# Performance work log

Measured on AMD Instinct MI355X. Metric: run time of the kernel, lower is better.

The kernel has to match this reference:

```python
import jax, jax.numpy as jnp
import numpy as np

BS, SL, ENC_DIM, EDGE_DIM = 8, 256, 1024, 256
MINUS_INF = -1.0e8


def setup_inputs() -> dict:
    key = jax.random.key(0)
    ks = jax.random.split(key, 5)
    encoded_text = jax.random.normal(ks[0], (BS, SL, ENC_DIM), dtype=jnp.float32)
    mask = jnp.ones((BS, SL), dtype=jnp.int64)
    # Linear params (torch stores weight as (out, in)); scale like default init
    Wh = jax.random.normal(ks[1], (EDGE_DIM, ENC_DIM), dtype=jnp.float32) / np.sqrt(ENC_DIM)
    bh = jax.random.normal(ks[2], (EDGE_DIM,), dtype=jnp.float32) / np.sqrt(ENC_DIM)
    Wc = jax.random.normal(ks[3], (EDGE_DIM, ENC_DIM), dtype=jnp.float32) / np.sqrt(ENC_DIM)
    w_out = jax.random.normal(ks[4], (EDGE_DIM,), dtype=jnp.float32) / np.sqrt(EDGE_DIM)
    return {"encoded_text": encoded_text, "mask": mask, "Wh": Wh, "bh": bh, "Wc": Wc, "w_out": w_out}


def reference(encoded_text, mask, Wh, bh, Wc, w_out):
    # head/child projections: (bs, sl, edge_dim)
    head = jnp.einsum('bse,de->bsd', encoded_text, Wh) + bh
    child = jnp.einsum('bse,de->bsd', encoded_text, Wc)
    # Pairwise: torch code gives combined[b,i,j] = tanh(head[b,j] + child[b,i])
    combined = jnp.tanh(head[:, None, :, :] + child[:, :, None, :])  # (bs, sl, sl, edge_dim)
    edge_scores = jnp.einsum('bijd,d->bij', combined, w_out)  # (bs, sl, sl)
    float_mask = mask.astype(jnp.float32)
    minus_mask = (1.0 - float_mask) * MINUS_INF  # (bs, sl)
    edge_scores = edge_scores + minus_mask[:, :, None] + minus_mask[:, None, :]
    return edge_scores
```

## Files before the change

kernel.cpp:

```cpp
#include <hip/hip_runtime.h>
#include <hip/hip_bf16.h>
#include <stdint.h>


typedef __bf16 bf16_t;
typedef __attribute__((ext_vector_type(8))) __bf16 bf16x8;
typedef __attribute__((ext_vector_type(4))) float f32x4;

#define SL 256
#define ENC 1024
#define NTOT 512
#define N_ENC 2097152
#define N_W 262144
#define KSCALE 2.8853900817779268f

__device__ __forceinline__ void async16(void* lds, const void* g) {
  __builtin_amdgcn_global_load_lds(
      (const __attribute__((address_space(1))) uint32_t*)g,
      (__attribute__((address_space(3))) uint32_t*)lds, 16, 0, 0);
}
__device__ __forceinline__ unsigned short f32_to_bf16_rne(float f) {
  uint32_t u = __float_as_uint(f);
  return (unsigned short)((u + 0x7FFFu + ((u >> 16) & 1u)) >> 16);
}

__global__ __launch_bounds__(256)
void convert_kernel(const float* __restrict__ enc, const float* __restrict__ Wh,
                    const float* __restrict__ Wc,
                    unsigned short* __restrict__ encB, unsigned short* __restrict__ WB) {
  int gi = (blockIdx.x * 256 + threadIdx.x) * 4;
  const float* src;
  unsigned short* dst;
  int off;
  if (gi < N_ENC) {
    src = enc; off = gi; dst = encB + gi;
  } else if (gi < N_ENC + N_W) {
    src = Wh; off = gi - N_ENC; dst = WB + off;
  } else {
    src = Wc; off = gi - N_ENC - N_W; dst = WB + N_W + off;
  }
  f32x4 v = *(const f32x4*)(src + off);
  ushort4 o;
  o.x = f32_to_bf16_rne(v[0]); o.y = f32_to_bf16_rne(v[1]);
  o.z = f32_to_bf16_rne(v[2]); o.w = f32_to_bf16_rne(v[3]);
  *(ushort4*)dst = o;
}

__global__ __launch_bounds__(256)
void proj_kernel(const unsigned short* __restrict__ A, const unsigned short* __restrict__ WB,
                 const float* __restrict__ bh, float* __restrict__ hc) {
  __shared__ bf16_t As[2][64 * 32];
  __shared__ bf16_t Bs[2][64 * 32];
  const int t = threadIdx.x;
  const int wv = t >> 6, lane = t & 63;
  const int m0 = blockIdx.x * 64;
  const int n0 = blockIdx.y * 64;
  const int srow = t >> 2, schunk = t & 3;
  const int mq = (wv & 1) * 32, nq = (wv >> 1) * 32;
  const int fr = lane & 15, kq = lane >> 4;

  f32x4 acc00 = {0.f, 0.f, 0.f, 0.f};
  f32x4 acc01 = acc00, acc10 = acc00, acc11 = acc00;

  const unsigned short* gA = A + (size_t)(m0 + srow) * ENC + schunk * 8;
  const unsigned short* gB = WB + (size_t)(n0 + srow) * ENC + schunk * 8;

  async16(&As[0][wv * 512], gA);
  async16(&Bs[0][wv * 512], gB);

#pragma unroll 4
  for (int i = 0; i < 32; ++i) {
    const int buf = i & 1;
    __syncthreads();
    if (i + 1 < 32) {
      const int k1 = (i + 1) * 32;
      async16(&As[buf ^ 1][wv * 512], gA + k1);
      async16(&Bs[buf ^ 1][wv * 512], gB + k1);
    }
    bf16x8 a0 = *(const bf16x8*)&As[buf][(mq + fr) * 32 + kq * 8];
    bf16x8 a1 = *(const bf16x8*)&As[buf][(mq + 16 + fr) * 32 + kq * 8];
    bf16x8 b0 = *(const bf16x8*)&Bs[buf][(nq + fr) * 32 + kq * 8];
    bf16x8 b1 = *(const bf16x8*)&Bs[buf][(nq + 16 + fr) * 32 + kq * 8];
    acc00 = __builtin_amdgcn_mfma_f32_16x16x32_bf16(a0, b0, acc00, 0, 0, 0);
    acc01 = __builtin_amdgcn_mfma_f32_16x16x32_bf16(a0, b1, acc01, 0, 0, 0);
    acc10 = __builtin_amdgcn_mfma_f32_16x16x32_bf16(a1, b0, acc10, 0, 0, 0);
    acc11 = __builtin_amdgcn_mfma_f32_16x16x32_bf16(a1, b1, acc11, 0, 0, 0);
  }
  const int colA = n0 + nq + fr;
  const int colB = colA + 16;
  const float biasA = (colA < 256) ? bh[colA] : 0.0f;
  const float biasB = (colB < 256) ? bh[colB] : 0.0f;
#pragma unroll
  for (int r = 0; r < 4; ++r) {
    int row0 = m0 + mq + kq * 4 + r;
    int row1 = row0 + 16;
    hc[(size_t)row0 * NTOT + colA] = __builtin_amdgcn_exp2f(KSCALE * (acc00[r] + biasA));
    hc[(size_t)row0 * NTOT + colB] = __builtin_amdgcn_exp2f(KSCALE * (acc01[r] + biasB));
    hc[(size_t)row1 * NTOT + colA] = __builtin_amdgcn_exp2f(KSCALE * (acc10[r] + biasA));
    hc[(size_t)row1 * NTOT + colB] = __builtin_amdgcn_exp2f(KSCALE * (acc11[r] + biasB));
  }
}

#define LSTR 260
__global__ __launch_bounds__(256)
void edge_kernel(const float* __restrict__ hc, const float* __restrict__ wout,
                 const int* __restrict__ mask, float* __restrict__ out) {
  __shared__ float ldH[32 * LSTR];
  __shared__ float ldC[32 * LSTR];
  __shared__ float wS[256];
  __shared__ float red[256];
  const int t = threadIdx.x;
  const int b = blockIdx.z;
  const int i0 = blockIdx.y * 32;
  const int j0 = blockIdx.x * 32;
  const int sbase = b * SL;

  float w = wout[t];
  wS[t] = -2.0f * w;
  red[t] = w;

  for (int u = t; u < 32 * 64; u += 256) {
    int row = u >> 6;
    int c4 = (u & 63) << 2;
    f32x4 hv = *(const f32x4*)&hc[(size_t)(sbase + j0 + row) * NTOT + c4];
    f32x4 cv = *(const f32x4*)&hc[(size_t)(sbase + i0 + row) * NTOT + 256 + c4];
    *(f32x4*)&ldH[row * LSTR + c4] = hv;
    *(f32x4*)&ldC[row * LSTR + c4] = cv;
  }
  __syncthreads();
  for (int s = 128; s > 0; s >>= 1) {
    if (t < s) red[t] += red[t + s];
    __syncthreads();
  }
  const float S = red[0];

  const int tx = t & 15, ty = t >> 4;
  const float* hp0 = &ldH[tx * LSTR];
  const float* hp1 = &ldH[(tx + 16) * LSTR];
  const float* cp0 = &ldC[ty * LSTR];
  const float* cp1 = &ldC[(ty + 16) * LSTR];
  float a00 = 0.f, a01 = 0.f, a10 = 0.f, a11 = 0.f;

#pragma unroll 8
  for (int d = 0; d < 256; d += 4) {
    f32x4 h0 = *(const f32x4*)&hp0[d];
    f32x4 h1 = *(const f32x4*)&hp1[d];
    f32x4 c0 = *(const f32x4*)&cp0[d];
    f32x4 c1 = *(const f32x4*)&cp1[d];
    f32x4 w4 = *(const f32x4*)&wS[d];
#pragma unroll
    for (int e = 0; e < 4; ++e) {
      float he0 = h0[e], he1 = h1[e], ce0 = c0[e], ce1 = c1[e], we = w4[e];
      float r00 = __builtin_amdgcn_rcpf(ce0 * he0 + 1.0f);
      float r01 = __builtin_amdgcn_rcpf(ce0 * he1 + 1.0f);
      float r10 = __builtin_amdgcn_rcpf(ce1 * he0 + 1.0f);
      float r11 = __builtin_amdgcn_rcpf(ce1 * he1 + 1.0f);
      a00 = fmaf(we, r00, a00);
      a01 = fmaf(we, r01, a01);
      a10 = fmaf(we, r10, a10);
      a11 = fmaf(we, r11, a11);
    }
  }

  const int gi0 = sbase + i0 + ty, gi1 = gi0 + 16;
  const int gj0 = j0 + tx, gj1 = gj0 + 16;
  const float mi0 = (1.0f - (float)mask[gi0]) * -1.0e8f;
  const float mi1 = (1.0f - (float)mask[gi1]) * -1.0e8f;
  const float mj0 = (1.0f - (float)mask[sbase + gj0]) * -1.0e8f;
  const float mj1 = (1.0f - (float)mask[sbase + gj1]) * -1.0e8f;
  out[(size_t)gi0 * SL + gj0] = S + a00 + mi0 + mj0;
  out[(size_t)gi0 * SL + gj1] = S + a01 + mi0 + mj1;
  out[(size_t)gi1 * SL + gj0] = S + a10 + mi1 + mj0;
  out[(size_t)gi1 * SL + gj1] = S + a11 + mi1 + mj1;
}

extern "C" void kernel_launch(void* const* d_in, const int* in_sizes, int n_in,
                              void* d_out, int out_size, void* d_ws, size_t ws_size,
                              hipStream_t stream) {
  (void)in_sizes; (void)n_in; (void)out_size; (void)ws_size;
  const float* enc = (const float*)d_in[0];
  const int* mask = (const int*)d_in[1];
  const float* Wh = (const float*)d_in[2];
  const float* bh = (const float*)d_in[3];
  const float* Wc = (const float*)d_in[4];
  const float* wout = (const float*)d_in[5];
  float* out = (float*)d_out;

  char* W = (char*)d_ws;
  float* hc = (float*)W;
  unsigned short* encB = (unsigned short*)(W + (4 << 20));
  unsigned short* WB = (unsigned short*)(W + (8 << 20));

  convert_kernel<<<2560, 256, 0, stream>>>(enc, Wh, Wc, encB, WB);
  proj_kernel<<<dim3(32, 8), 256, 0, stream>>>(encB, WB, bh, hc);
  edge_kernel<<<dim3(8, 8, 8), 256, 0, stream>>>(hc, wout, mask, out);
}
```

Measured before the change: 104.1 us.

## Fuse convert, projection and edge kernels into one cooperative launch

Result: slower. 202.9 us (+94.8%).

```diff
diff --git a/kernel.cpp b/kernel.cpp
--- a/kernel.cpp
+++ b/kernel.cpp
@@ -1,7 +1,10 @@
 #include <hip/hip_runtime.h>
 #include <hip/hip_bf16.h>
+#include <hip/hip_cooperative_groups.h>
 #include <stdint.h>
 
+
+namespace cg = cooperative_groups;
 
 typedef __bf16 bf16_t;
 typedef __attribute__((ext_vector_type(8))) __bf16 bf16x8;
@@ -13,6 +16,7 @@
 #define N_ENC 2097152
 #define N_W 262144
 #define KSCALE 2.8853900817779268f
+#define LSTR 260
 
 __device__ __forceinline__ void async16(void* lds, const void* g) {
   __builtin_amdgcn_global_load_lds(
@@ -22,6 +26,161 @@
 __device__ __forceinline__ unsigned short f32_to_bf16_rne(float f) {
   uint32_t u = __float_as_uint(f);
   return (unsigned short)((u + 0x7FFFu + ((u >> 16) & 1u)) >> 16);
+}
+
+union SMem {
+  struct { bf16_t As[2][2048]; bf16_t Bs[2][2048]; } p;
+  struct { float ldH[32 * LSTR]; float ldC[32 * LSTR]; float wS[256]; float red[256]; } e;
+};
+
+__global__ __launch_bounds__(256)
+void fused_coop(const float* __restrict__ enc, const int* __restrict__ mask,
+                const float* __restrict__ Wh, const float* __restrict__ bh,
+                const float* __restrict__ Wc, const float* __restrict__ wout,
+                float* __restrict__ hc, unsigned short* __restrict__ encB,
+                unsigned short* __restrict__ WB, float* __restrict__ out) {
+  __shared__ SMem sm;
+  cg::grid_group grid = cg::this_grid();
+  const int bid = blockIdx.x;
+  const int t = threadIdx.x;
+
+#pragma unroll
+  for (int k = 0; k < 10; ++k) {
+    int gi = ((bid * 256 + t) + k * 65536) * 4;
+    const float* src;
+    unsigned short* dst;
+    int off;
+    if (gi < N_ENC) {
+      src = enc; off = gi; dst = encB + gi;
+    } else if (gi < N_ENC + N_W) {
+      src = Wh; off = gi - N_ENC; dst = WB + off;
+    } else {
+      src = Wc; off = gi - N_ENC - N_W; dst = WB + N_W + off;
+    }
+    f32x4 v = *(const f32x4*)(src + off);
+    ushort4 o;
+    o.x = f32_to_bf16_rne(v[0]); o.y = f32_to_bf16_rne(v[1]);
+    o.z = f32_to_bf16_rne(v[2]); o.w = f32_to_bf16_rne(v[3]);
+    *(ushort4*)dst = o;
+  }
+  grid.sync();
+
+  {
+    const int wv = t >> 6, lane = t & 63;
+    const int m0 = (bid & 31) * 64;
+    const int n0 = (bid >> 5) * 64;
+    const int srow = t >> 2, schunk = t & 3;
+    const int mq = (wv & 1) * 32, nq = (wv >> 1) * 32;
+    const int fr = lane & 15, kq = lane >> 4;
+
+    f32x4 acc00 = {0.f, 0.f, 0.f, 0.f};
+    f32x4 acc01 = acc00, acc10 = acc00, acc11 = acc00;
+
+    const unsigned short* gA = encB + (size_t)(m0 + srow) * ENC + schunk * 8;
+    const unsigned short* gB = WB + (size_t)(n0 + srow) * ENC + schunk * 8;
+
+    async16(&sm.p.As[0][wv * 512], gA);
+    async16(&sm.p.Bs[0][wv * 512], gB);
+
+#pragma unroll 4
+    for (int i = 0; i < 32; ++i) {
+      const int buf = i & 1;
+      __syncthreads();
+      if (i + 1 < 32) {
+        const int k1 = (i + 1) * 32;
+        async16(&sm.p.As[buf ^ 1][wv * 512], gA + k1);
+        async16(&sm.p.Bs[buf ^ 1][wv * 512], gB + k1);
+      }
+      bf16x8 a0 = *(const bf16x8*)&sm.p.As[buf][(mq + fr) * 32 + kq * 8];
+      bf16x8 a1 = *(const bf16x8*)&sm.p.As[buf][(mq + 16 + fr) * 32 + kq * 8];
+      bf16x8 b0 = *(const bf16x8*)&sm.p.Bs[buf][(nq + fr) * 32 + kq * 8];
+      bf16x8 b1 = *(const bf16x8*)&sm.p.Bs[buf][(nq + 16 + fr) * 32 + kq * 8];
+      acc00 = __builtin_amdgcn_mfma_f32_16x16x32_bf16(a0, b0, acc00, 0, 0, 0);
+      acc01 = __builtin_amdgcn_mfma_f32_16x16x32_bf16(a0, b1, acc01, 0, 0, 0);
+      acc10 = __builtin_amdgcn_mfma_f32_16x16x32_bf16(a1, b0, acc10, 0, 0, 0);
+      acc11 = __builtin_amdgcn_mfma_f32_16x16x32_bf16(a1, b1, acc11, 0, 0, 0);
+    }
+    const int colA = n0 + nq + fr;
+    const int colB = colA + 16;
+    const float biasA = (colA < 256) ? bh[colA] : 0.0f;
+    const float biasB = (colB < 256) ? bh[colB] : 0.0f;
+#pragma unroll
+    for (int r = 0; r < 4; ++r) {
+      int row0 = m0 + mq + kq * 4 + r;
+      int row1 = row0 + 16;
+      hc[(size_t)row0 * NTOT + colA] = __builtin_amdgcn_exp2f(KSCALE * (acc00[r] + biasA));
+      hc[(size_t)row0 * NTOT + colB] = __builtin_amdgcn_exp2f(KSCALE * (acc01[r] + biasB));
+      hc[(size_t)row1 * NTOT + colA] = __builtin_amdgcn_exp2f(KSCALE * (acc10[r] + biasA));
+      hc[(size_t)row1 * NTOT + colB] = __builtin_amdgcn_exp2f(KSCALE * (acc11[r] + biasB));
+    }
+  }
+  grid.sync();
+
+  for (int tile = bid; tile < 512; tile += 256) {
+    __syncthreads();
+    const int b = tile >> 6;
+    const int i0 = ((tile >> 3) & 7) * 32;
+    const int j0 = (tile & 7) * 32;
+    const int sbase = b * SL;
+
+    float w = wout[t];
+    sm.e.wS[t] = -2.0f * w;
+    sm.e.red[t] = w;
+
+    for (int u = t; u < 32 * 64; u += 256) {
+      int row = u >> 6;
+      int c4 = (u & 63) << 2;
+      f32x4 hv = *(const f32x4*)&hc[(size_t)(sbase + j0 + row) * NTOT + c4];
+      f32x4 cv = *(const f32x4*)&hc[(size_t)(sbase + i0 + row) * NTOT + 256 + c4];
+      *(f32x4*)&sm.e.ldH[row * LSTR + c4] = hv;
+      *(f32x4*)&sm.e.ldC[row * LSTR + c4] = cv;
+    }
+    __syncthreads();
+    for (int s = 128; s > 0; s >>= 1) {
+      if (t < s) sm.e.red[t] += sm.e.red[t + s];
+      __syncthreads();
+    }
+    const float S = sm.e.red[0];
+
+    const int tx = t & 15, ty = t >> 4;
+    const float* hp0 = &sm.e.ldH[tx * LSTR];
+    const float* hp1 = &sm.e.ldH[(tx + 16) * LSTR];
+    const float* cp0 = &sm.e.ldC[ty * LSTR];
+    const float* cp1 = &sm.e.ldC[(ty + 16) * LSTR];
+    float a00 = 0.f, a01 = 0.f, a10 = 0.f, a11 = 0.f;
+
+#pragma unroll 8
+    for (int d = 0; d < 256; d += 4) {
+      f32x4 h0 = *(const f32x4*)&hp0[d];
+      f32x4 h1 = *(const f32x4*)&hp1[d];
+      f32x4 c0 = *(const f32x4*)&cp0[d];
+      f32x4 c1 = *(const f32x4*)&cp1[d];
+      f32x4 w4 = *(const f32x4*)&sm.e.wS[d];
+#pragma unroll
+      for (int e = 0; e < 4; ++e) {
+        float he0 = h0[e], he1 = h1[e], ce0 = c0[e], ce1 = c1[e], we = w4[e];
+        float r00 = __builtin_amdgcn_rcpf(ce0 * he0 + 1.0f);
+        float r01 = __builtin_amdgcn_rcpf(ce0 * he1 + 1.0f);
+        float r10 = __builtin_amdgcn_rcpf(ce1 * he0 + 1.0f);
+        float r11 = __builtin_amdgcn_rcpf(ce1 * he1 + 1.0f);
+        a00 = fmaf(we, r00, a00);
+        a01 = fmaf(we, r01, a01);
+        a10 = fmaf(we, r10, a10);
+        a11 = fmaf(we, r11, a11);
+      }
+    }
+
+    const int gi0 = sbase + i0 + ty, gi1 = gi0 + 16;
+    const int gj0 = j0 + tx, gj1 = gj0 + 16;
+    const float mi0 = (1.0f - (float)mask[gi0]) * -1.0e8f;
+    const float mi1 = (1.0f - (float)mask[gi1]) * -1.0e8f;
+    const float mj0 = (1.0f - (float)mask[sbase + gj0]) * -1.0e8f;
+    const float mj1 = (1.0f - (float)mask[sbase + gj1]) * -1.0e8f;
+    out[(size_t)gi0 * SL + gj0] = S + a00 + mi0 + mj0;
+    out[(size_t)gi0 * SL + gj1] = S + a01 + mi0 + mj1;
+    out[(size_t)gi1 * SL + gj0] = S + a10 + mi1 + mj0;
+    out[(size_t)gi1 * SL + gj1] = S + a11 + mi1 + mj1;
+  }
 }
 
 __global__ __launch_bounds__(256)
@@ -32,13 +191,9 @@
   const float* src;
   unsigned short* dst;
   int off;
-  if (gi < N_ENC) {
-    src = enc; off = gi; dst = encB + gi;
-  } else if (gi < N_ENC + N_W) {
-    src = Wh; off = gi - N_ENC; dst = WB + off;
-  } else {
-    src = Wc; off = gi - N_ENC - N_W; dst = WB + N_W + off;
-  }
+  if (gi < N_ENC) { src = enc; off = gi; dst = encB + gi; }
+  else if (gi < N_ENC + N_W) { src = Wh; off = gi - N_ENC; dst = WB + off; }
+  else { src = Wc; off = gi - N_ENC - N_W; dst = WB + N_W + off; }
   f32x4 v = *(const f32x4*)(src + off);
   ushort4 o;
   o.x = f32_to_bf16_rne(v[0]); o.y = f32_to_bf16_rne(v[1]);
@@ -58,16 +213,12 @@
   const int srow = t >> 2, schunk = t & 3;
   const int mq = (wv & 1) * 32, nq = (wv >> 1) * 32;
   const int fr = lane & 15, kq = lane >> 4;
-
   f32x4 acc00 = {0.f, 0.f, 0.f, 0.f};
   f32x4 acc01 = acc00, acc10 = acc00, acc11 = acc00;
-
   const unsigned short* gA = A + (size_t)(m0 + srow) * ENC + schunk * 8;
   const unsigned short* gB = WB + (size_t)(n0 + srow) * ENC + schunk * 8;
-
   async16(&As[0][wv * 512], gA);
   async16(&Bs[0][wv * 512], gB);
-
 #pragma unroll 4
   for (int i = 0; i < 32; ++i) {
     const int buf = i & 1;
@@ -101,7 +252,6 @@
   }
 }
 
-#define LSTR 260
 __global__ __launch_bounds__(256)
 void edge_kernel(const float* __restrict__ hc, const float* __restrict__ wout,
                  const int* __restrict__ mask, float* __restrict__ out) {
@@ -114,11 +264,9 @@
   const int i0 = blockIdx.y * 32;
   const int j0 = blockIdx.x * 32;
   const int sbase = b * SL;
-
   float w = wout[t];
   wS[t] = -2.0f * w;
   red[t] = w;
-
   for (int u = t; u < 32 * 64; u += 256) {
     int row = u >> 6;
     int c4 = (u & 63) << 2;
@@ -133,14 +281,12 @@
     __syncthreads();
   }
   const float S = red[0];
-
   const int tx = t & 15, ty = t >> 4;
   const float* hp0 = &ldH[tx * LSTR];
   const float* hp1 = &ldH[(tx + 16) * LSTR];
   const float* cp0 = &ldC[ty * LSTR];
   const float* cp1 = &ldC[(ty + 16) * LSTR];
   float a00 = 0.f, a01 = 0.f, a10 = 0.f, a11 = 0.f;
-
 #pragma unroll 8
   for (int d = 0; d < 256; d += 4) {
     f32x4 h0 = *(const f32x4*)&hp0[d];
@@ -161,7 +307,6 @@
       a11 = fmaf(we, r11, a11);
     }
   }
-
   const int gi0 = sbase + i0 + ty, gi1 = gi0 + 16;
   const int gj0 = j0 + tx, gj1 = gj0 + 16;
   const float mi0 = (1.0f - (float)mask[gi0]) * -1.0e8f;
@@ -191,7 +336,14 @@
   unsigned short* encB = (unsigned short*)(W + (4 << 20));
   unsigned short* WB = (unsigned short*)(W + (8 << 20));
 
-  convert_kernel<<<2560, 256, 0, stream>>>(enc, Wh, Wc, encB, WB);
-  proj_kernel<<<dim3(32, 8), 256, 0, stream>>>(encB, WB, bh, hc);
-  edge_kernel<<<dim3(8, 8, 8), 256, 0, stream>>>(hc, wout, mask, out);
-}
+  void* args[] = {(void*)&enc, (void*)&mask, (void*)&Wh, (void*)&bh,
+                  (void*)&Wc, (void*)&wout, (void*)&hc, (void*)&encB,
+                  (void*)&WB, (void*)&out};
+  hipError_t err = hipLaunchCooperativeKernel((const void*)fused_coop,
+                                              dim3(256), dim3(256), args, 0, stream);
+  if (err != hipSuccess) {
+    convert_kernel<<<2560, 256, 0, stream>>>(enc, Wh, Wc, encB, WB);
+    proj_kernel<<<dim3(32, 8), 256, 0, stream>>>(encB, WB, bh, hc);
+    edge_kernel<<<dim3(8, 8, 8), 256, 0, stream>>>(hc, wout, mask, out);
+  }
+}
```
